# Performance work log

Measured on AMD Instinct MI355X. Metric: run time of the kernel, lower is better.

Reference implementation:

```python
import jax, jax.numpy as jnp
import numpy as np

D_MODEL = 512
N_HEADS = 8
D_K = D_MODEL // N_HEADS
B, L_Q, L_K = 4, 2048, 2048


def setup_inputs() -> dict:
    key = jax.random.key(0)
    ks = jax.random.split(key, 13)
    s = 1.0 / np.sqrt(D_MODEL)
    return {
        "Q_in": jax.random.normal(ks[0], (B, L_Q, D_MODEL), jnp.float32),
        "K_in": jax.random.normal(ks[1], (B, L_K, D_MODEL), jnp.float32),
        "V_in": jax.random.normal(ks[2], (B, L_K, D_MODEL), jnp.float32),
        "M": jax.random.uniform(ks[3], (N_HEADS, L_Q, L_K), jnp.float32),
        "Wq": jax.random.uniform(ks[4], (D_MODEL, D_MODEL), jnp.float32, -s, s),
        "bq": jnp.zeros((D_MODEL,), jnp.float32),
        "Wk": jax.random.uniform(ks[5], (D_MODEL, D_MODEL), jnp.float32, -s, s),
        "bk": jnp.zeros((D_MODEL,), jnp.float32),
        "Wv": jax.random.uniform(ks[6], (D_MODEL, D_MODEL), jnp.float32, -s, s),
        "bv": jnp.zeros((D_MODEL,), jnp.float32),
        "Wo": jax.random.uniform(ks[7], (D_MODEL, D_MODEL), jnp.float32, -s, s),
        "bo": jnp.zeros((D_MODEL,), jnp.float32),
        "logit_alpha": jnp.zeros((N_HEADS,), jnp.float32),
    }


def reference(Q_in, K_in, V_in, M, Wq, bq, Wk, bk, Wv, bv, Wo, bo, logit_alpha):
    b, lq, _ = Q_in.shape
    lk = K_in.shape[1]
    # projections (torch Linear: x @ W.T + b), split into heads: [b, h, l, d_k]
    Q = (Q_in @ Wq.T + bq).reshape(b, lq, N_HEADS, D_K).transpose(0, 2, 1, 3)
    K = (K_in @ Wk.T + bk).reshape(b, lk, N_HEADS, D_K).transpose(0, 2, 1, 3)
    V = (V_in @ Wv.T + bv).reshape(b, lk, N_HEADS, D_K).transpose(0, 2, 1, 3)
    logits = jnp.einsum("bhqd,bhkd->bhqk", Q, K) / jnp.sqrt(jnp.asarray(D_K, Q.dtype))
    attn = jax.nn.softmax(logits, axis=-1)
    alpha = jax.nn.sigmoid(logit_alpha)[None, :, None, None]  # [1, h, 1, 1]
    gate = alpha * M[None] + (1.0 - alpha)  # post-softmax soft-mask gate
    attn = attn * gate
    out = jnp.einsum("bhqk,bhkd->bqhd", attn, V).reshape(b, lq, D_MODEL)
    return out @ Wo.T + bo, attn
```

## Files before the change

kernel.cpp:

```cpp
#include <hip/hip_runtime.h>
#include <hip/hip_bf16.h>

typedef unsigned short u16;
typedef unsigned int u32;
typedef short bf16x8 __attribute__((ext_vector_type(8)));
typedef float f32x4 __attribute__((ext_vector_type(4)));
typedef u16 u16x8 __attribute__((ext_vector_type(8)));
typedef u16 u16x4 __attribute__((ext_vector_type(4)));
typedef u32 u32x2 __attribute__((ext_vector_type(2)));

#define WQ_ 0
#define WK_ 262144
#define WV_ 524288
#define WO_ 786432
#define QP_ 1048576
#define KP_ (QP_ + 4194304)
#define VT_ (KP_ + 4194304)
#define OW_ (VT_ + 4194304)

#define C1F 0.18033688011112042f

__device__ __forceinline__ u16 f2bf(float f) {
  unsigned x = __float_as_uint(f);
  return (u16)((x + 0x7fffu + ((x >> 16) & 1u)) >> 16);
}

__device__ __forceinline__ u32 packbf2(float a, float b) {
  u32 lo = (u32)__bfloat16_as_ushort(__float2bfloat16(a));
  u32 hi = (u32)__bfloat16_as_ushort(__float2bfloat16(b));
  return lo | (hi << 16);
}

__device__ __forceinline__ void async16(const void* g, void* l) {
  __builtin_amdgcn_global_load_lds(
      (const __attribute__((address_space(1))) unsigned int*)g,
      (__attribute__((address_space(3))) unsigned int*)l, 16, 0, 0);
}

__global__ void convert_w(const float* __restrict__ Wq, const float* __restrict__ Wk,
                          const float* __restrict__ Wv, const float* __restrict__ Wo,
                          u16* __restrict__ ws) {
  int seg = blockIdx.y;
  const float* src = (seg == 0) ? Wq : (seg == 1) ? Wk : (seg == 2) ? Wv : Wo;
  u16* dst = ws + seg * 262144;
  int i = (blockIdx.x * 256 + threadIdx.x) * 8;
  float4 a = *(const float4*)(src + i);
  float4 b = *(const float4*)(src + i + 4);
  u16x8 o;
  o[0] = f2bf(a.x); o[1] = f2bf(a.y); o[2] = f2bf(a.z); o[3] = f2bf(a.w);
  o[4] = f2bf(b.x); o[5] = f2bf(b.y); o[6] = f2bf(b.z); o[7] = f2bf(b.w);
  *(u16x8*)(dst + i) = o;
}

template <int MODE>
__global__ __launch_bounds__(256, 3) void gemm_nt(
    const float* __restrict__ A0, const float* __restrict__ A1,
    const float* __restrict__ A2, u16* __restrict__ ws,
    const float* __restrict__ bias0, const float* __restrict__ bias1,
    const float* __restrict__ bias2, float* __restrict__ outF) {
  const int tid = threadIdx.x, lane = tid & 63, wave = tid >> 6;
  const int wm = wave >> 1, wn = wave & 1;
  const int z = blockIdx.z;
  const float* Af = (z == 0) ? A0 : (z == 1) ? A1 : A2;
  const u16* W = ws + (MODE == 0 ? z * 262144 : (int)WO_);
  const u16* Ab = ws + OW_;
  const float* bias = (z == 0) ? bias0 : (z == 1) ? bias1 : bias2;
  const int bm0 = blockIdx.y * 128, bn0 = blockIdx.x * 128;

  __shared__ u16 At[8192];
  __shared__ u16 Bt[8192];

  f32x4 acc[4][4];
#pragma unroll
  for (int i = 0; i < 4; ++i)
#pragma unroll
    for (int j = 0; j < 4; ++j) acc[i][j] = (f32x4){0.f, 0.f, 0.f, 0.f};

  const int grp16 = (lane >> 4) * 16;

  for (int kt = 0; kt < 8; ++kt) {
    __syncthreads();
#pragma unroll
    for (int c = 0; c < 4; ++c) {
      int o = wave * 4096 + c * 1024 + lane * 16;
      int row = o >> 7;
      int colb = (o & 127) ^ ((row & 7) << 4);
      async16((const char*)W + (size_t)(bn0 + row) * 1024 + kt * 128 + colb,
              (char*)Bt + wave * 4096 + c * 1024);
      if (MODE == 1) {
        async16((const char*)Ab + (size_t)(bm0 + row) * 1024 + kt * 128 + colb,
                (char*)At + wave * 4096 + c * 1024);
      }
    }
    if (MODE == 0) {
#pragma unroll
      for (int i = 0; i < 4; ++i) {
        int c = tid + 256 * i;
        int row = c >> 3, fc = (c & 7) * 8;
        const float* s = Af + (size_t)(bm0 + row) * 512 + kt * 64 + fc;
        f32x4 x0 = *(const f32x4*)s;
        f32x4 x1 = *(const f32x4*)(s + 4);
        u16x8 p;
        p[0] = __bfloat16_as_ushort(__float2bfloat16(x0[0]));
        p[1] = __bfloat16_as_ushort(__float2bfloat16(x0[1]));
        p[2] = __bfloat16_as_ushort(__float2bfloat16(x0[2]));
        p[3] = __bfloat16_as_ushort(__float2bfloat16(x0[3]));
        p[4] = __bfloat16_as_ushort(__float2bfloat16(x1[0]));
        p[5] = __bfloat16_as_ushort(__float2bfloat16(x1[1]));
        p[6] = __bfloat16_as_ushort(__float2bfloat16(x1[2]));
        p[7] = __bfloat16_as_ushort(__float2bfloat16(x1[3]));
        int db = row * 128 + ((fc * 2) ^ ((row & 7) << 4));
        *(u16x8*)((char*)At + db) = p;
      }
    }
    __syncthreads();
    bf16x8 af[4][2], bfr[4][2];
#pragma unroll
    for (int rb = 0; rb < 4; ++rb) {
      int row = wm * 64 + rb * 16 + (lane & 15);
      const char* base = (const char*)At + row * 128;
      int sw = (row & 7) << 4;
      af[rb][0] = *(const bf16x8*)(base + (grp16 ^ sw));
      af[rb][1] = *(const bf16x8*)(base + ((64 + grp16) ^ sw));
    }
#pragma unroll
    for (int cb = 0; cb < 4; ++cb) {
      int row = wn * 64 + cb * 16 + (lane & 15);
      const char* base = (const char*)Bt + row * 128;
      int sw = (row & 7) << 4;
      bfr[cb][0] = *(const bf16x8*)(base + (grp16 ^ sw));
      bfr[cb][1] = *(const bf16x8*)(base + ((64 + grp16) ^ sw));
    }
#pragma unroll
    for (int rb = 0; rb < 4; ++rb)
#pragma unroll
      for (int cb = 0; cb < 4; ++cb) {
        acc[rb][cb] = __builtin_amdgcn_mfma_f32_16x16x32_bf16(af[rb][0], bfr[cb][0],
                                                              acc[rb][cb], 0, 0, 0);
        acc[rb][cb] = __builtin_amdgcn_mfma_f32_16x16x32_bf16(af[rb][1], bfr[cb][1],
                                                              acc[rb][cb], 0, 0, 0);
      }
  }

#pragma unroll
  for (int rb = 0; rb < 4; ++rb) {
#pragma unroll
    for (int cb = 0; cb < 4; ++cb) {
      int col = bn0 + wn * 64 + cb * 16 + (lane & 15);
      float bvl = bias[col];
#pragma unroll
      for (int r = 0; r < 4; ++r) {
        int rr = bm0 + wm * 64 + rb * 16 + (lane >> 4) * 4 + r;
        float v = acc[rb][cb][r] + bvl;
        if (MODE == 1) {
          outF[(size_t)rr * 512 + col] = v;
        } else {
          int b = rr >> 11, q = rr & 2047, hh = col >> 6, dd = col & 63;
          int bh = (b << 3) | hh;
          if (z == 0) {
            ws[QP_ + (size_t)(bh * 2048 + q) * 64 + dd] = f2bf(v * C1F);
          } else if (z == 1) {
            ws[KP_ + (size_t)(bh * 2048 + q) * 64 + dd] = f2bf(v);
          } else {
            ws[VT_ + (size_t)bh * 131072 + (size_t)dd * 2048 + q] = f2bf(v);
          }
        }
      }
    }
  }
}

__global__ __launch_bounds__(256, 4) void attn_kernel(u16* __restrict__ ws,
                                                      const float* __restrict__ Mg,
                                                      const float* __restrict__ la,
                                                      float* __restrict__ attnOut) {
  const int tid = threadIdx.x, lane = tid & 63, wv = tid >> 6;
  const int colLane = lane & 15, grp = lane >> 4;
  const int yb = blockIdx.y, h = yb >> 2, b = yb & 3, bh = b * 8 + h;
  const int q0 = blockIdx.x * 32;
  const u16* Qp = ws + QP_ + (size_t)bh * 131072;
  const u16* Kp = ws + KP_ + (size_t)bh * 131072;
  const u16* Vtg = ws + VT_ + (size_t)bh * 131072;
  const float* Mh = Mg + (size_t)h * 4194304;
  float alpha = 1.f / (1.f + __expf(-la[h]));
  float oma = 1.f - alpha;

  __shared__ u16 pool[16640];
  char* Kw = (char*)pool + wv * 8192;
  char* Vw = Kw + 4096;
  float* Zbuf = (float*)((char*)pool + 32768);

  bf16x8 qf[2][2];
#pragma unroll
  for (int qb = 0; qb < 2; ++qb)
#pragma unroll
    for (int dh = 0; dh < 2; ++dh)
      qf[qb][dh] = *(const bf16x8*)(Qp + (size_t)(q0 + qb * 16 + colLane) * 64 +
                                    dh * 32 + grp * 8);

  auto stageK = [&](int t) {
#pragma unroll
    for (int c = 0; c < 4; ++c) {
      int o = c * 1024 + lane * 16;
      int row = o >> 7;
      int colb = (o & 127) ^ ((row & 7) << 4);
      async16((const char*)Kp + (size_t)(t * 128 + wv * 32 + row) * 128 + colb,
              Kw + o);
    }
  };
  auto stageV = [&](int t) {
#pragma unroll
    for (int c = 0; c < 4; ++c) {
      int o = c * 1024 + lane * 16;
      int d = o >> 6;
      int slot = (o >> 4) & 3;
      int ks = (slot ^ (d & 3)) * 8;
      async16((const char*)Vtg + ((size_t)d * 2048 + t * 128 + wv * 32 + ks) * 2,
              Vw + o);
    }
  };
  auto qk = [&](float sc[2][2][4]) {
    bf16x8 kf[2][2];
#pragma unroll
    for (int kb = 0; kb < 2; ++kb) {
      int row = kb * 16 + colLane;
      int sw = (row & 7) << 4;
#pragma unroll
      for (int dh = 0; dh < 2; ++dh)
        kf[kb][dh] = *(const bf16x8*)(Kw + row * 128 + ((dh * 64 + grp * 16) ^ sw));
    }
    __builtin_amdgcn_s_setprio(1);
#pragma unroll
    for (int kb = 0; kb < 2; ++kb)
#pragma unroll
      for (int qb = 0; qb < 2; ++qb) {
        f32x4 a = (f32x4){0.f, 0.f, 0.f, 0.f};
        a = __builtin_amdgcn_mfma_f32_16x16x32_bf16(kf[kb][0], qf[qb][0], a, 0, 0, 0);
        a = __builtin_amdgcn_mfma_f32_16x16x32_bf16(kf[kb][1], qf[qb][1], a, 0, 0, 0);
#pragma unroll
        for (int r = 0; r < 4; ++r) sc[kb][qb][r] = a[r];
      }
    __builtin_amdgcn_s_setprio(0);
  };

  float zp0 = 0.f, zp1 = 0.f;
  for (int t = 0; t < 16; ++t) {
    asm volatile("s_waitcnt lgkmcnt(0)" ::: "memory");
    stageK(t);
    asm volatile("s_waitcnt vmcnt(0)" ::: "memory");
    float sc[2][2][4];
    qk(sc);
#pragma unroll
    for (int kb = 0; kb < 2; ++kb)
#pragma unroll
      for (int r = 0; r < 4; ++r) {
        zp0 += exp2f(sc[kb][0][r]);
        zp1 += exp2f(sc[kb][1][r]);
      }
  }
  zp0 += __shfl_xor(zp0, 16); zp0 += __shfl_xor(zp0, 32);
  zp1 += __shfl_xor(zp1, 16); zp1 += __shfl_xor(zp1, 32);
  if (lane < 16) {
    Zbuf[wv * 32 + lane] = zp0;
    Zbuf[wv * 32 + 16 + lane] = zp1;
  }
  __syncthreads();
  float aZ[2], oZ[2];
#pragma unroll
  for (int qb = 0; qb < 2; ++qb) {
    float z = Zbuf[qb * 16 + colLane] + Zbuf[32 + qb * 16 + colLane] +
              Zbuf[64 + qb * 16 + colLane] + Zbuf[96 + qb * 16 + colLane];
    float iz = 1.f / z;
    aZ[qb] = alpha * iz;
    oZ[qb] = oma * iz;
  }

  f32x4 oacc[4][2];
#pragma unroll
  for (int db = 0; db < 4; ++db)
#pragma unroll
    for (int qb = 0; qb < 2; ++qb) oacc[db][qb] = (f32x4){0.f, 0.f, 0.f, 0.f};

  const float* Mrow[2];
  float* Arow[2];
#pragma unroll
  for (int qb = 0; qb < 2; ++qb) {
    int qg = q0 + qb * 16 + colLane;
    Mrow[qb] = Mh + (size_t)qg * 2048 + wv * 32 + grp * 4;
    Arow[qb] = attnOut + ((size_t)(bh * 2048 + qg)) * 2048 + wv * 32 + grp * 4;
  }
  char* Pb = Kw;

  for (int t = 0; t < 16; ++t) {
    float4 mreg[2][2];
#pragma unroll
    for (int qb = 0; qb < 2; ++qb)
#pragma unroll
      for (int kb = 0; kb < 2; ++kb)
        mreg[kb][qb] = *(const float4*)(Mrow[qb] + t * 128 + kb * 16);
    asm volatile("s_waitcnt lgkmcnt(0)" ::: "memory");
    stageK(t);
    stageV(t);
    asm volatile("s_waitcnt vmcnt(0)" ::: "memory");
    float sc[2][2][4];
    qk(sc);
#pragma unroll
    for (int kb = 0; kb < 2; ++kb)
#pragma unroll
      for (int qb = 0; qb < 2; ++qb) {
        f32x4 uv;
        uv[0] = exp2f(sc[kb][qb][0]) * fmaf(aZ[qb], mreg[kb][qb].x, oZ[qb]);
        uv[1] = exp2f(sc[kb][qb][1]) * fmaf(aZ[qb], mreg[kb][qb].y, oZ[qb]);
        uv[2] = exp2f(sc[kb][qb][2]) * fmaf(aZ[qb], mreg[kb][qb].z, oZ[qb]);
        uv[3] = exp2f(sc[kb][qb][3]) * fmaf(aZ[qb], mreg[kb][qb].w, oZ[qb]);
        __builtin_nontemporal_store(uv, (f32x4*)(Arow[qb] + t * 128 + kb * 16));
        u32x2 pv;
        pv[0] = packbf2(uv[0], uv[1]);
        pv[1] = packbf2(uv[2], uv[3]);
        *(u32x2*)(Pb + qb * 1280 + colLane * 80 + kb * 32 + grp * 8) = pv;
      }
    bf16x8 pf[2];
#pragma unroll
    for (int qb = 0; qb < 2; ++qb)
      pf[qb] = *(const bf16x8*)(Pb + qb * 1280 + colLane * 80 + grp * 16);
    __builtin_amdgcn_s_setprio(1);
#pragma unroll
    for (int db = 0; db < 4; ++db) {
      int d = db * 16 + colLane;
      bf16x8 vf = *(const bf16x8*)(Vw + d * 64 + ((grp * 16) ^ ((d & 3) << 4)));
#pragma unroll
      for (int qb = 0; qb < 2; ++qb)
        oacc[db][qb] = __builtin_amdgcn_mfma_f32_16x16x32_bf16(vf, pf[qb],
                                                               oacc[db][qb], 0, 0, 0);
    }
    __builtin_amdgcn_s_setprio(0);
  }

  __syncthreads();
  float* Ob = (float*)pool;
#pragma unroll
  for (int db = 0; db < 4; ++db)
#pragma unroll
    for (int qb = 0; qb < 2; ++qb) {
      *(f32x4*)((char*)Ob + wv * 8192 + (qb * 16 + colLane) * 256 +
                (db * 16 + grp * 4) * 4) = oacc[db][qb];
    }
  __syncthreads();
#pragma unroll
  for (int j = 0; j < 2; ++j) {
    int idx = tid * 8 + j * 4;
    int q = idx >> 6, d = idx & 63;
    f32x4 s = *(const f32x4*)((char*)Ob + q * 256 + d * 4);
#pragma unroll
    for (int w = 1; w < 4; ++w) {
      f32x4 sw2 = *(const f32x4*)((char*)Ob + w * 8192 + q * 256 + d * 4);
      s[0] += sw2[0]; s[1] += sw2[1]; s[2] += sw2[2]; s[3] += sw2[3];
    }
    u16x4 ov;
    ov[0] = f2bf(s[0]); ov[1] = f2bf(s[1]); ov[2] = f2bf(s[2]); ov[3] = f2bf(s[3]);
    *(u16x4*)(ws + OW_ + (size_t)(b * 2048 + q0 + q) * 512 + h * 64 + d) = ov;
  }
}

extern "C" void kernel_launch(void* const* d_in, const int* in_sizes, int n_in,
                              void* d_out, int out_size, void* d_ws, size_t ws_size,
                              hipStream_t stream) {
  const float* Qi = (const float*)d_in[0];
  const float* Ki = (const float*)d_in[1];
  const float* Vi = (const float*)d_in[2];
  const float* M = (const float*)d_in[3];
  const float* Wq = (const float*)d_in[4];
  const float* bq = (const float*)d_in[5];
  const float* Wk = (const float*)d_in[6];
  const float* bk = (const float*)d_in[7];
  const float* Wv = (const float*)d_in[8];
  const float* bv = (const float*)d_in[9];
  const float* Wo = (const float*)d_in[10];
  const float* bo = (const float*)d_in[11];
  const float* la = (const float*)d_in[12];
  u16* ws = (u16*)d_ws;
  float* outMain = (float*)d_out;
  float* outAttn = outMain + 4194304;

  convert_w<<<dim3(128, 4), 256, 0, stream>>>(Wq, Wk, Wv, Wo, ws);
  gemm_nt<0><<<dim3(4, 64, 3), 256, 0, stream>>>(Qi, Ki, Vi, ws, bq, bk, bv, nullptr);
  attn_kernel<<<dim3(64, 32), 256, 0, stream>>>(ws, M, la, outAttn);
  gemm_nt<1><<<dim3(4, 64, 1), 256, 0, stream>>>(nullptr, nullptr, nullptr, ws, bo,
                                                 nullptr, nullptr, outMain);
}
```

Baseline: 250.2 us.

## Register-prefetch K/V tiles in attention and halve output GEMM M-tile

The attention kernel stops using async global-to-LDS copies followed by full vmcnt waits. It now loads the next K/V tile into registers while computing on the current one, then writes those registers into swizzled LDS at the start of the next iteration, which overlaps global latency with the QK and PV math. Separately, the output projection GEMM uses 64-row M tiles with twice as many blocks, for better CU occupancy on a small problem. The prefetch adds register pressure under launch bounds of 4, and the explicit waitcnt removal relies on compiler-inserted waits for correctness within each wave.

```diff
diff --git a/kernel.cpp b/kernel.cpp
--- a/kernel.cpp
+++ b/kernel.cpp
@@ -8,6 +8,7 @@
 typedef u16 u16x8 __attribute__((ext_vector_type(8)));
 typedef u16 u16x4 __attribute__((ext_vector_type(4)));
 typedef u32 u32x2 __attribute__((ext_vector_type(2)));
+typedef u32 u32x4 __attribute__((ext_vector_type(4)));
 
 #define WQ_ 0
 #define WK_ 262144
@@ -58,6 +59,8 @@
     const float* __restrict__ A2, u16* __restrict__ ws,
     const float* __restrict__ bias0, const float* __restrict__ bias1,
     const float* __restrict__ bias2, float* __restrict__ outF) {
+  constexpr int MT = (MODE == 0) ? 128 : 64;
+  constexpr int RB = MT / 32;
   const int tid = threadIdx.x, lane = tid & 63, wave = tid >> 6;
   const int wm = wave >> 1, wn = wave & 1;
   const int z = blockIdx.z;
@@ -65,14 +68,14 @@
   const u16* W = ws + (MODE == 0 ? z * 262144 : (int)WO_);
   const u16* Ab = ws + OW_;
   const float* bias = (z == 0) ? bias0 : (z == 1) ? bias1 : bias2;
-  const int bm0 = blockIdx.y * 128, bn0 = blockIdx.x * 128;
-
-  __shared__ u16 At[8192];
+  const int bm0 = blockIdx.y * MT, bn0 = blockIdx.x * 128;
+
+  __shared__ u16 At[MT * 64];
   __shared__ u16 Bt[8192];
 
-  f32x4 acc[4][4];
-#pragma unroll
-  for (int i = 0; i < 4; ++i)
+  f32x4 acc[RB][4];
+#pragma unroll
+  for (int i = 0; i < RB; ++i)
 #pragma unroll
     for (int j = 0; j < 4; ++j) acc[i][j] = (f32x4){0.f, 0.f, 0.f, 0.f};
 
@@ -87,9 +90,15 @@
       int colb = (o & 127) ^ ((row & 7) << 4);
       async16((const char*)W + (size_t)(bn0 + row) * 1024 + kt * 128 + colb,
               (char*)Bt + wave * 4096 + c * 1024);
-      if (MODE == 1) {
+    }
+    if (MODE == 1) {
+#pragma unroll
+      for (int c = 0; c < RB; ++c) {
+        int o = wave * (MT * 32) + c * 1024 + lane * 16;
+        int row = o >> 7;
+        int colb = (o & 127) ^ ((row & 7) << 4);
         async16((const char*)Ab + (size_t)(bm0 + row) * 1024 + kt * 128 + colb,
-                (char*)At + wave * 4096 + c * 1024);
+                (char*)At + wave * (MT * 32) + c * 1024);
       }
     }
     if (MODE == 0) {
@@ -114,10 +123,10 @@
       }
     }
     __syncthreads();
-    bf16x8 af[4][2], bfr[4][2];
-#pragma unroll
-    for (int rb = 0; rb < 4; ++rb) {
-      int row = wm * 64 + rb * 16 + (lane & 15);
+    bf16x8 af[RB][2], bfr[4][2];
+#pragma unroll
+    for (int rb = 0; rb < RB; ++rb) {
+      int row = wm * (MT / 2) + rb * 16 + (lane & 15);
       const char* base = (const char*)At + row * 128;
       int sw = (row & 7) << 4;
       af[rb][0] = *(const bf16x8*)(base + (grp16 ^ sw));
@@ -132,7 +141,7 @@
       bfr[cb][1] = *(const bf16x8*)(base + ((64 + grp16) ^ sw));
     }
 #pragma unroll
-    for (int rb = 0; rb < 4; ++rb)
+    for (int rb = 0; rb < RB; ++rb)
 #pragma unroll
       for (int cb = 0; cb < 4; ++cb) {
         acc[rb][cb] = __builtin_amdgcn_mfma_f32_16x16x32_bf16(af[rb][0], bfr[cb][0],
@@ -143,14 +152,14 @@
   }
 
 #pragma unroll
-  for (int rb = 0; rb < 4; ++rb) {
+  for (int rb = 0; rb < RB; ++rb) {
 #pragma unroll
     for (int cb = 0; cb < 4; ++cb) {
       int col = bn0 + wn * 64 + cb * 16 + (lane & 15);
       float bvl = bias[col];
 #pragma unroll
       for (int r = 0; r < 4; ++r) {
-        int rr = bm0 + wm * 64 + rb * 16 + (lane >> 4) * 4 + r;
+        int rr = bm0 + wm * (MT / 2) + rb * 16 + (lane >> 4) * 4 + r;
         float v = acc[rb][cb][r] + bvl;
         if (MODE == 1) {
           outF[(size_t)rr * 512 + col] = v;
@@ -179,8 +188,8 @@
   const int yb = blockIdx.y, h = yb >> 2, b = yb & 3, bh = b * 8 + h;
   const int q0 = blockIdx.x * 32;
   const u16* Qp = ws + QP_ + (size_t)bh * 131072;
-  const u16* Kp = ws + KP_ + (size_t)bh * 131072;
-  const u16* Vtg = ws + VT_ + (size_t)bh * 131072;
+  const char* Kg = (const char*)(ws + KP_ + (size_t)bh * 131072);
+  const char* Vg = (const char*)(ws + VT_ + (size_t)bh * 131072);
   const float* Mh = Mg + (size_t)h * 4194304;
   float alpha = 1.f / (1.f + __expf(-la[h]));
   float oma = 1.f - alpha;
@@ -198,25 +207,38 @@
       qf[qb][dh] = *(const bf16x8*)(Qp + (size_t)(q0 + qb * 16 + colLane) * 64 +
                                     dh * 32 + grp * 8);
 
-  auto stageK = [&](int t) {
+  auto loadK = [&](int t, u32x4 kr[4]) {
 #pragma unroll
     for (int c = 0; c < 4; ++c) {
       int o = c * 1024 + lane * 16;
       int row = o >> 7;
-      int colb = (o & 127) ^ ((row & 7) << 4);
-      async16((const char*)Kp + (size_t)(t * 128 + wv * 32 + row) * 128 + colb,
-              Kw + o);
+      kr[c] = *(const u32x4*)(Kg + (size_t)(t * 128 + wv * 32 + row) * 128 +
+                              (o & 127));
     }
   };
-  auto stageV = [&](int t) {
+  auto loadV = [&](int t, u32x4 vr[4]) {
 #pragma unroll
     for (int c = 0; c < 4; ++c) {
       int o = c * 1024 + lane * 16;
       int d = o >> 6;
-      int slot = (o >> 4) & 3;
-      int ks = (slot ^ (d & 3)) * 8;
-      async16((const char*)Vtg + ((size_t)d * 2048 + t * 128 + wv * 32 + ks) * 2,
-              Vw + o);
+      vr[c] = *(const u32x4*)(Vg + (size_t)d * 4096 + (size_t)(t * 128 + wv * 32) * 2 +
+                              (o & 63));
+    }
+  };
+  auto writeK = [&](const u32x4 kr[4]) {
+#pragma unroll
+    for (int c = 0; c < 4; ++c) {
+      int o = c * 1024 + lane * 16;
+      int row = o >> 7;
+      *(u32x4*)(Kw + row * 128 + ((o & 127) ^ ((row & 7) << 4))) = kr[c];
+    }
+  };
+  auto writeV = [&](const u32x4 vr[4]) {
+#pragma unroll
+    for (int c = 0; c < 4; ++c) {
+      int o = c * 1024 + lane * 16;
+      int d = o >> 6;
+      *(u32x4*)(Vw + d * 64 + ((o & 63) ^ ((d & 3) << 4))) = vr[c];
     }
   };
   auto qk = [&](float sc[2][2][4]) {
@@ -243,11 +265,12 @@
     __builtin_amdgcn_s_setprio(0);
   };
 
+  u32x4 kr[4];
+  loadK(0, kr);
   float zp0 = 0.f, zp1 = 0.f;
   for (int t = 0; t < 16; ++t) {
-    asm volatile("s_waitcnt lgkmcnt(0)" ::: "memory");
-    stageK(t);
-    asm volatile("s_waitcnt vmcnt(0)" ::: "memory");
+    writeK(kr);
+    if (t < 15) loadK(t + 1, kr);
     float sc[2][2][4];
     qk(sc);
 #pragma unroll
@@ -291,17 +314,19 @@
   }
   char* Pb = Kw;
 
+  u32x4 vr[4];
+  loadK(0, kr);
+  loadV(0, vr);
   for (int t = 0; t < 16; ++t) {
+    writeK(kr);
+    writeV(vr);
+    if (t < 15) { loadK(t + 1, kr); loadV(t + 1, vr); }
     float4 mreg[2][2];
 #pragma unroll
     for (int qb = 0; qb < 2; ++qb)
 #pragma unroll
       for (int kb = 0; kb < 2; ++kb)
         mreg[kb][qb] = *(const float4*)(Mrow[qb] + t * 128 + kb * 16);
-    asm volatile("s_waitcnt lgkmcnt(0)" ::: "memory");
-    stageK(t);
-    stageV(t);
-    asm volatile("s_waitcnt vmcnt(0)" ::: "memory");
     float sc[2][2][4];
     qk(sc);
 #pragma unroll
@@ -385,6 +410,6 @@
   convert_w<<<dim3(128, 4), 256, 0, stream>>>(Wq, Wk, Wv, Wo, ws);
   gemm_nt<0><<<dim3(4, 64, 3), 256, 0, stream>>>(Qi, Ki, Vi, ws, bq, bk, bv, nullptr);
   attn_kernel<<<dim3(64, 32), 256, 0, stream>>>(ws, M, la, outAttn);
-  gemm_nt<1><<<dim3(4, 64, 1), 256, 0, stream>>>(nullptr, nullptr, nullptr, ws, bo,
-                                                 nullptr, nullptr, outMain);
-}
+  gemm_nt<1><<<dim3(4, 128, 1), 256, 0, stream>>>(nullptr, nullptr, nullptr, ws, bo,
+                                                  nullptr, nullptr, outMain);
+}
```

Measured after the change: 576.6 us. 130% more time.
